# Performance work log

Measured on AMD Instinct MI355X. Metric: run time of the kernel, lower is better.

## Reference

```python
import jax, jax.numpy as jnp
import numpy as np

D_N = 128  # node_embedding_dimensions
D_E = 128  # edge_embedding_dimensions
N_REL = 1000  # edge_count (number of relations)
BATCH = 16384


def _l2_normalize(x, eps=1e-12):
    # mimics torch.nn.functional.normalize(p=2, dim=1)
    norm = jnp.sqrt(jnp.sum(x * x, axis=1, keepdims=True))
    return x / jnp.maximum(norm, eps)


def setup_inputs() -> dict:
    key = jax.random.key(0)
    k1, k2, k3, k4, k5 = jax.random.split(key, 5)
    head_embeddings = jax.random.normal(k1, (BATCH, D_N), dtype=jnp.float32)
    tail_embeddings = jax.random.normal(k2, (BATCH, D_N), dtype=jnp.float32)
    edge_embeddings = jax.random.normal(k3, (BATCH, D_E), dtype=jnp.float32)
    proj_table = jax.random.normal(k4, (N_REL, D_E * D_N), dtype=jnp.float32)
    edge_indices = jax.random.randint(k5, (BATCH,), 0, N_REL, dtype=jnp.int64)
    return {
        "head_embeddings": head_embeddings,
        "tail_embeddings": tail_embeddings,
        "edge_embeddings": edge_embeddings,
        "proj_table": proj_table,
        "edge_indices": edge_indices,
    }


def reference(head_embeddings, tail_embeddings, edge_embeddings, proj_table, edge_indices):
    # L2-normalize head/tail node embeddings along feature dim
    h = _l2_normalize(head_embeddings)  # [B, d_n]
    t = _l2_normalize(tail_embeddings)  # [B, d_n]
    B = h.shape[0]
    # gather per-relation projection matrices: [B, d_e, d_n]
    P = proj_table[edge_indices].reshape(B, D_E, D_N)
    # project heads/tails into relation space: matmul(P, x[...,None]) -> [B, d_e]
    ph = jnp.einsum("bed,bd->be", P, h)
    pt = jnp.einsum("bed,bd->be", P, t)
    # l2 dissimilarity: squared L2 norm of (h_proj + r - t_proj); score is its negation
    diff = ph + edge_embeddings - pt
    return -jnp.sum(diff * diff, axis=1)
```

## Files before the change

### kernel.cpp

```cpp
#include <hip/hip_runtime.h>
#include <stdint.h>

#define D 128
#define LIST_CAP 256

#define SMEM_FLOATS (16384 + 1024 + 1024 + 16 + LIST_CAP + 8 + 1)
#define SMEM_BYTES (SMEM_FLOATS * 4)

__global__ __launch_bounds__(512, 4) void transr_fused(
    const float* __restrict__ head,
    const float* __restrict__ tail,
    const float* __restrict__ edge,
    const float* __restrict__ proj,
    const int* __restrict__ idx,
    float* __restrict__ out,
    int B)
{
    const int rel = blockIdx.x;
    const int tid = threadIdx.x;

    extern __shared__ float sm[];
    float* Pl   = sm;
    float* Ul   = sm + 16384;
    float* Rl   = sm + 17408;
    float* part = sm + 18432;
    int*   list = (int*)(sm + 18448);
    int*   El   = (int*)(sm + 18704);
    int*   cnt  = (int*)(sm + 18712);

    if (tid == 0) *cnt = 0;

    const float* __restrict__ Pg = proj + (size_t)rel * (D * D);
    #pragma unroll
    for (int i = 0; i < 8; ++i) {
        const int f   = i * 512 + tid;
        const int row = f >> 5;
        const int q   = f & 31;
        const float* src = Pg + row * D + 4 * (q ^ (row & 31));
        float* dst = Pl + 4 * f;
        __builtin_amdgcn_global_load_lds(
            (const __attribute__((address_space(1))) uint32_t*)src,
            (__attribute__((address_space(3))) uint32_t*)dst,
            16, 0, 0);
    }

    __syncthreads();

    const int4* __restrict__ idx4 = reinterpret_cast<const int4*>(idx);
    const int nv = B >> 2;
    for (int f = tid; f < nv; f += 512) {
        const int4 v = idx4[f];
        if (v.x == rel) { int p = atomicAdd(cnt, 1); if (p < LIST_CAP) list[p] = 4 * f + 0; }
        if (v.y == rel) { int p = atomicAdd(cnt, 1); if (p < LIST_CAP) list[p] = 4 * f + 1; }
        if (v.z == rel) { int p = atomicAdd(cnt, 1); if (p < LIST_CAP) list[p] = 4 * f + 2; }
        if (v.w == rel) { int p = atomicAdd(cnt, 1); if (p < LIST_CAP) list[p] = 4 * f + 3; }
    }
    __syncthreads();
    const int n = min(*cnt, LIST_CAP);
    if (n == 0) return;

    const int w    = tid >> 6;
    const int wl   = tid & 63;
    const int e0   = 2 * (w & 3);
    const int e1   = e0 + 1;
    const int half = w >> 2;
    const int row  = half * 64 + wl;
    const float* Prow = Pl + row * D;
    const int sx = wl & 31;

    const int nchunk = (n + 7) >> 3;
    for (int ch = 0; ch < nchunk; ++ch) {
        const int e = ch * 8 + w;
        int b = -1;
        float2 u2 = make_float2(0.f, 0.f);
        float2 r2 = make_float2(0.f, 0.f);
        if (e < n) {
            b = list[e];
            const float2 h2 = *reinterpret_cast<const float2*>(head + (size_t)b * D + 2 * wl);
            const float2 t2 = *reinterpret_cast<const float2*>(tail + (size_t)b * D + 2 * wl);
            r2 = *reinterpret_cast<const float2*>(edge + (size_t)b * D + 2 * wl);
            float hs = h2.x * h2.x + h2.y * h2.y;
            float ts = t2.x * t2.x + t2.y * t2.y;
            #pragma unroll
            for (int m = 1; m < 64; m <<= 1) {
                hs += __shfl_xor(hs, m);
                ts += __shfl_xor(ts, m);
            }
            const float hn = fmaxf(sqrtf(hs), 1e-12f);
            const float tn = fmaxf(sqrtf(ts), 1e-12f);
            u2.x = h2.x / hn - t2.x / tn;
            u2.y = h2.y / hn - t2.y / tn;
        }
        *reinterpret_cast<float2*>(Ul + w * D + 2 * wl) = u2;
        *reinterpret_cast<float2*>(Rl + w * D + 2 * wl) = r2;
        if (wl == 0) El[w] = b;
        __syncthreads();

        float acc0 = 0.f, acc1 = 0.f;
        const float* U0 = Ul + e0 * D;
        const float* U1 = Ul + e1 * D;
        #pragma unroll
        for (int q = 0; q < 32; ++q) {
            const float4 p = *reinterpret_cast<const float4*>(Prow + 4 * (q ^ sx));
            const float4 a = *reinterpret_cast<const float4*>(U0 + 4 * q);
            const float4 c = *reinterpret_cast<const float4*>(U1 + 4 * q);
            acc0 = fmaf(p.x, a.x, acc0); acc0 = fmaf(p.y, a.y, acc0);
            acc0 = fmaf(p.z, a.z, acc0); acc0 = fmaf(p.w, a.w, acc0);
            acc1 = fmaf(p.x, c.x, acc1); acc1 = fmaf(p.y, c.y, acc1);
            acc1 = fmaf(p.z, c.z, acc1); acc1 = fmaf(p.w, c.w, acc1);
        }
        const float d0 = acc0 + Rl[e0 * D + row];
        const float d1 = acc1 + Rl[e1 * D + row];
        float s0 = d0 * d0;
        float s1 = d1 * d1;
        #pragma unroll
        for (int m = 1; m < 64; m <<= 1) {
            s0 += __shfl_xor(s0, m);
            s1 += __shfl_xor(s1, m);
        }
        if (wl == 0) {
            part[half * 8 + e0] = s0;
            part[half * 8 + e1] = s1;
        }
        __syncthreads();

        if (tid < 8) {
            const int bb = El[tid];
            if (bb >= 0) out[bb] = -(part[tid] + part[8 + tid]);
        }
        __syncthreads();
    }
}

extern "C" void kernel_launch(void* const* d_in, const int* in_sizes, int n_in,
                              void* d_out, int out_size, void* d_ws, size_t ws_size,
                              hipStream_t stream) {
    const float* head = (const float*)d_in[0];
    const float* tail = (const float*)d_in[1];
    const float* edge = (const float*)d_in[2];
    const float* proj = (const float*)d_in[3];
    const int*   idx  = (const int*)d_in[4];
    float* out = (float*)d_out;

    const int B    = in_sizes[0] / D;
    const int nrel = in_sizes[3] / (D * D);

    hipFuncSetAttribute(reinterpret_cast<const void*>(transr_fused),
                        hipFuncAttributeMaxDynamicSharedMemorySize, SMEM_BYTES);
    transr_fused<<<nrel, 512, SMEM_BYTES, stream>>>(head, tail, edge, proj,
                                                    idx, out, B);
}
```

Baseline: 146.6 us.

## Hold projection slices in registers and reduce partial dot products via LDS atomics

```diff
diff --git a/kernel.cpp b/kernel.cpp
--- a/kernel.cpp
+++ b/kernel.cpp
@@ -4,7 +4,7 @@
 #define D 128
 #define LIST_CAP 256
 
-#define SMEM_FLOATS (16384 + 1024 + 1024 + 16 + LIST_CAP + 8 + 1)
+#define SMEM_FLOATS (16384 + 1024 + 1024 + 1024 + LIST_CAP + 8 + 1)
 #define SMEM_BYTES (SMEM_FLOATS * 4)
 
 __global__ __launch_bounds__(512, 4) void transr_fused(
@@ -24,11 +24,13 @@
     float* Ul   = sm + 16384;
     float* Rl   = sm + 17408;
     float* part = sm + 18432;
-    int*   list = (int*)(sm + 18448);
-    int*   El   = (int*)(sm + 18704);
-    int*   cnt  = (int*)(sm + 18712);
+    int*   list = (int*)(sm + 19456);
+    int*   El   = (int*)(sm + 19456 + LIST_CAP);
+    int*   cnt  = El + 8;
 
     if (tid == 0) *cnt = 0;
+    part[tid] = 0.f;
+    part[tid + 512] = 0.f;
 
     const float* __restrict__ Pg = proj + (size_t)rel * (D * D);
     #pragma unroll
@@ -59,14 +61,21 @@
     const int n = min(*cnt, LIST_CAP);
     if (n == 0) return;
 
-    const int w    = tid >> 6;
-    const int wl   = tid & 63;
-    const int e0   = 2 * (w & 3);
-    const int e1   = e0 + 1;
-    const int half = w >> 2;
-    const int row  = half * 64 + wl;
-    const float* Prow = Pl + row * D;
+    const int w  = tid >> 6;
+    const int wl = tid & 63;
+    const int cq = w & 3;
+    const int eh = w >> 2;
+    const int rowA = wl;
+    const int rowB = wl + 64;
     const int sx = wl & 31;
+
+    float4 pA[8], pB[8];
+    #pragma unroll
+    for (int k = 0; k < 8; ++k) {
+        const int ql = 8 * cq + k;
+        pA[k] = *reinterpret_cast<const float4*>(Pl + rowA * D + 4 * (ql ^ sx));
+        pB[k] = *reinterpret_cast<const float4*>(Pl + rowB * D + 4 * (ql ^ sx));
+    }
 
     const int nchunk = (n + 7) >> 3;
     for (int ch = 0; ch < nchunk; ++ch) {
@@ -96,37 +105,38 @@
         if (wl == 0) El[w] = b;
         __syncthreads();
 
-        float acc0 = 0.f, acc1 = 0.f;
-        const float* U0 = Ul + e0 * D;
-        const float* U1 = Ul + e1 * D;
         #pragma unroll
-        for (int q = 0; q < 32; ++q) {
-            const float4 p = *reinterpret_cast<const float4*>(Prow + 4 * (q ^ sx));
-            const float4 a = *reinterpret_cast<const float4*>(U0 + 4 * q);
-            const float4 c = *reinterpret_cast<const float4*>(U1 + 4 * q);
-            acc0 = fmaf(p.x, a.x, acc0); acc0 = fmaf(p.y, a.y, acc0);
-            acc0 = fmaf(p.z, a.z, acc0); acc0 = fmaf(p.w, a.w, acc0);
-            acc1 = fmaf(p.x, c.x, acc1); acc1 = fmaf(p.y, c.y, acc1);
-            acc1 = fmaf(p.z, c.z, acc1); acc1 = fmaf(p.w, c.w, acc1);
-        }
-        const float d0 = acc0 + Rl[e0 * D + row];
-        const float d1 = acc1 + Rl[e1 * D + row];
-        float s0 = d0 * d0;
-        float s1 = d1 * d1;
-        #pragma unroll
-        for (int m = 1; m < 64; m <<= 1) {
-            s0 += __shfl_xor(s0, m);
-            s1 += __shfl_xor(s1, m);
-        }
-        if (wl == 0) {
-            part[half * 8 + e0] = s0;
-            part[half * 8 + e1] = s1;
+        for (int j = 0; j < 4; ++j) {
+            const int e2 = eh * 4 + j;
+            const float* Ue = Ul + e2 * D + 32 * cq;
+            float a0 = 0.f, a1 = 0.f;
+            #pragma unroll
+            for (int k = 0; k < 8; ++k) {
+                const float4 u = *reinterpret_cast<const float4*>(Ue + 4 * k);
+                a0 = fmaf(pA[k].x, u.x, a0); a0 = fmaf(pA[k].y, u.y, a0);
+                a0 = fmaf(pA[k].z, u.z, a0); a0 = fmaf(pA[k].w, u.w, a0);
+                a1 = fmaf(pB[k].x, u.x, a1); a1 = fmaf(pB[k].y, u.y, a1);
+                a1 = fmaf(pB[k].z, u.z, a1); a1 = fmaf(pB[k].w, u.w, a1);
+            }
+            atomicAdd(&part[e2 * D + rowA], a0);
+            atomicAdd(&part[e2 * D + rowB], a1);
         }
         __syncthreads();
 
-        if (tid < 8) {
-            const int bb = El[tid];
-            if (bb >= 0) out[bb] = -(part[tid] + part[8 + tid]);
+        {
+            const float p0 = part[w * D + wl];
+            const float p1 = part[w * D + wl + 64];
+            part[w * D + wl] = 0.f;
+            part[w * D + wl + 64] = 0.f;
+            const float d0 = p0 + Rl[w * D + wl];
+            const float d1 = p1 + Rl[w * D + wl + 64];
+            float s = fmaf(d0, d0, d1 * d1);
+            #pragma unroll
+            for (int m = 1; m < 64; m <<= 1) s += __shfl_xor(s, m);
+            if (wl == 0) {
+                const int bb = El[w];
+                if (bb >= 0) out[bb] = -s;
+            }
         }
         __syncthreads();
     }
```

Result: slower. 191.1 us (+30.3%).
